# Performance work log

Hardware: AMD Instinct MI355X
Metric: run time of the kernel (lower is better)

Reference implementation:

```python
import jax, jax.numpy as jnp
import numpy as np

# FreeConv2D: locally-connected 2D conv (unshared per-location kernels) + bias.
# out[b,oh,ow,u] = sum_{i,j,c} w[oh,ow,u,i,j,c] * x[b, oh*s1+i, ow*s2+j, c] + bias[oh,ow,u]

B, H, W, C = 64, 64, 64, 64
U, K, S = 64, 5, 2
OH = (H - K) // S + 1  # 30 (== ceil((H-K+1)/S))
OW = (W - K) // S + 1  # 30


def setup_inputs() -> dict:
    key = jax.random.key(0)
    kx, kw, kb = jax.random.split(key, 3)
    x = jax.random.normal(kx, (B, H, W, C), dtype=jnp.float32)
    w = jax.random.normal(kw, (OH, OW, U, K, K, C), dtype=jnp.float32) * 0.05
    b = jax.random.normal(kb, (OH, OW, U), dtype=jnp.float32) * 0.05
    return {"x": x, "w": w, "b": b}


def reference(x, w, b):
    s1 = s2 = S
    # Accumulate over the small fixed kernel window (K*K = 25 taps);
    # each tap is a per-location contraction over channels (batched GEMV).
    out = jnp.zeros((x.shape[0], OH, OW, U), dtype=x.dtype)
    for i in range(K):
        for j in range(K):
            # x_slice[b,oh,ow,c] = x[b, oh*s1+i, ow*s2+j, c]
            x_slice = x[:, i:i + (OH - 1) * s1 + 1:s1, j:j + (OW - 1) * s2 + 1:s2, :]
            out = out + jnp.einsum('bhwc,hwuc->bhwu', x_slice, w[:, :, :, i, j, :])
    return out + b  # activation is None (identity)
```

## Files before the change

kernel.cpp:

```cpp
#include <hip/hip_runtime.h>


typedef __bf16 bf16x8 __attribute__((ext_vector_type(8)));
typedef float f32x4 __attribute__((ext_vector_type(4)));

__device__ __forceinline__ unsigned short f2bf(float f) {
    unsigned int u = __float_as_uint(f);
    u += 0x7FFFu + ((u >> 16) & 1u);
    return (unsigned short)(u >> 16);
}


__global__ __launch_bounds__(256, 4)
void freeconv_kernel(const float* __restrict__ x,
                     const float* __restrict__ w,
                     const float* __restrict__ bias,
                     float* __restrict__ out) {
    __shared__ __align__(16) unsigned short ldsA[10240];
    __shared__ __align__(16) unsigned short ldsB[10240];

    const int bid = blockIdx.x;
    const int oh = bid / 30;
    const int ow = bid - oh * 30;
    const int t = threadIdx.x;
    const int lane = t & 63;
    const int wave = t >> 6;
    const int wm = wave >> 1;
    const int wn = wave & 1;

    const int swz = ((lane >> 4) << 7) + (((lane & 15) ^ (lane >> 4)) << 3);

    int rr[10], cc[10], ww[10];
#pragma unroll
    for (int it = 0; it < 10; ++it) {
        int g = it * 256 + t;
        int r = g / 40;
        int k = (g - r * 40) * 4;
        rr[it] = r;
        cc[it] = k;
        int grp = (k >> 3) & 3;
        ww[it] = ((k >> 5) * 4 + (r >> 4)) * 512 + grp * 128 + (((r & 15) ^ grp) * 8) + (k & 7);
    }

    f32x4 acc[2][2];
#pragma unroll
    for (int a = 0; a < 2; ++a)
#pragma unroll
        for (int b2 = 0; b2 < 2; ++b2)
#pragma unroll
            for (int r = 0; r < 4; ++r) acc[a][b2][r] = 0.f;

    const float* wblk = w + (oh * 30 + ow) * 102400;

    for (int ci = 0; ci < 10; ++ci) {
        const int i  = ci >> 1;
        const int kh = ci & 1;
        const int aoff = (oh * 2 + i) * 4096 + ow * 128 + kh * 160;
        const int boff = i * 320 + kh * 160;

#pragma unroll
        for (int bt = 0; bt < 2; ++bt) {
            float4 va[5], vb[5];
#pragma unroll
            for (int q = 0; q < 5; ++q) {
                int it = bt * 5 + q;
                va[q] = *(const float4*)(x + rr[it] * 262144 + aoff + cc[it]);
            }
#pragma unroll
            for (int q = 0; q < 5; ++q) {
                int it = bt * 5 + q;
                vb[q] = *(const float4*)(wblk + rr[it] * 1600 + boff + cc[it]);
            }
#pragma unroll
            for (int q = 0; q < 5; ++q) {
                int it = bt * 5 + q;
                ushort4 pv;
                pv.x = f2bf(va[q].x); pv.y = f2bf(va[q].y);
                pv.z = f2bf(va[q].z); pv.w = f2bf(va[q].w);
                *(ushort4*)&ldsA[ww[it]] = pv;
            }
#pragma unroll
            for (int q = 0; q < 5; ++q) {
                int it = bt * 5 + q;
                ushort4 pv;
                pv.x = f2bf(vb[q].x); pv.y = f2bf(vb[q].y);
                pv.z = f2bf(vb[q].z); pv.w = f2bf(vb[q].w);
                *(ushort4*)&ldsB[ww[it]] = pv;
            }
        }
        __syncthreads();

#pragma unroll
        for (int ks = 0; ks < 5; ++ks) {
            const bf16x8 a0 = *(const bf16x8*)&ldsA[(ks * 4 + wm * 2 + 0) * 512 + swz];
            const bf16x8 a1 = *(const bf16x8*)&ldsA[(ks * 4 + wm * 2 + 1) * 512 + swz];
            const bf16x8 b0 = *(const bf16x8*)&ldsB[(ks * 4 + wn * 2 + 0) * 512 + swz];
            const bf16x8 b1 = *(const bf16x8*)&ldsB[(ks * 4 + wn * 2 + 1) * 512 + swz];
            acc[0][0] = __builtin_amdgcn_mfma_f32_16x16x32_bf16(a0, b0, acc[0][0], 0, 0, 0);
            acc[0][1] = __builtin_amdgcn_mfma_f32_16x16x32_bf16(a0, b1, acc[0][1], 0, 0, 0);
            acc[1][0] = __builtin_amdgcn_mfma_f32_16x16x32_bf16(a1, b0, acc[1][0], 0, 0, 0);
            acc[1][1] = __builtin_amdgcn_mfma_f32_16x16x32_bf16(a1, b1, acc[1][1], 0, 0, 0);
        }
        __syncthreads();
    }

    const float* bp = bias + (oh * 30 + ow) * 64;
    const int col = lane & 15;
    const int r0 = (lane >> 4) * 4;
    float bv0 = bp[wn * 32 + col];
    float bv1 = bp[wn * 32 + 16 + col];
#pragma unroll
    for (int ms = 0; ms < 2; ++ms) {
#pragma unroll
        for (int r = 0; r < 4; ++r) {
            int bi = wm * 32 + ms * 16 + r0 + r;
            float* op = out + ((bi * 30 + oh) * 30 + ow) * 64 + wn * 32 + col;
            op[0]  = acc[ms][0][r] + bv0;
            op[16] = acc[ms][1][r] + bv1;
        }
    }
}

extern "C" void kernel_launch(void* const* d_in, const int* in_sizes, int n_in,
                              void* d_out, int out_size, void* d_ws, size_t ws_size,
                              hipStream_t stream) {
    const float* x = (const float*)d_in[0];
    const float* w = (const float*)d_in[1];
    const float* b = (const float*)d_in[2];
    float* out = (float*)d_out;
    (void)in_sizes; (void)n_in; (void)out_size; (void)d_ws; (void)ws_size;
    freeconv_kernel<<<dim3(900), dim3(256), 0, stream>>>(x, w, b, out);
}
```

Measured before the change: 565.8 us.

## Prefetch next weight chunk in registers and remap blocks across XCDs

Weight tiles for the next chunk are loaded into registers while the current chunk's activation tile is converted and stored, overlapping the weight stream (the dominant traffic) with LDS writes and MFMA work. Block indices are remapped so neighbouring output locations land on the same XCD, which should improve L2 reuse of the overlapping input windows. Per-thread LDS address arrays are recomputed inline instead of held in registers. The change adds register pressure (20 float4 live values) under a 4-block occupancy bound, which could cause spills.

```diff
diff --git a/kernel.cpp b/kernel.cpp
--- a/kernel.cpp
+++ b/kernel.cpp
@@ -10,6 +10,12 @@
     return (unsigned short)(u >> 16);
 }
 
+__device__ __forceinline__ ushort4 pk4(const float4 v) {
+    ushort4 p;
+    p.x = f2bf(v.x); p.y = f2bf(v.y); p.z = f2bf(v.z); p.w = f2bf(v.w);
+    return p;
+}
+
 
 __global__ __launch_bounds__(256, 4)
 void freeconv_kernel(const float* __restrict__ x,
@@ -19,7 +25,12 @@
     __shared__ __align__(16) unsigned short ldsA[10240];
     __shared__ __align__(16) unsigned short ldsB[10240];
 
-    const int bid = blockIdx.x;
+    const int orig = blockIdx.x;
+    const int xcd  = orig & 7;
+    const int idx  = orig >> 3;
+    const int bid  = (xcd < 4) ? (xcd * 113 + idx)
+                               : (452 + (xcd - 4) * 112 + idx);
+
     const int oh = bid / 30;
     const int ow = bid - oh * 30;
     const int t = threadIdx.x;
@@ -30,17 +41,10 @@
 
     const int swz = ((lane >> 4) << 7) + (((lane & 15) ^ (lane >> 4)) << 3);
 
-    int rr[10], cc[10], ww[10];
+    int rr[10];
 #pragma unroll
-    for (int it = 0; it < 10; ++it) {
-        int g = it * 256 + t;
-        int r = g / 40;
-        int k = (g - r * 40) * 4;
-        rr[it] = r;
-        cc[it] = k;
-        int grp = (k >> 3) & 3;
-        ww[it] = ((k >> 5) * 4 + (r >> 4)) * 512 + grp * 128 + (((r & 15) ^ grp) * 8) + (k & 7);
-    }
+    for (int q = 0; q < 10; ++q) rr[q] = (q * 256 + t) / 40;
+    const int t4 = t << 2;
 
     f32x4 acc[2][2];
 #pragma unroll
@@ -50,44 +54,54 @@
 #pragma unroll
             for (int r = 0; r < 4; ++r) acc[a][b2][r] = 0.f;
 
-    const float* wblk = w + (oh * 30 + ow) * 102400;
+    const float* wblk = w + (size_t)bid * 102400;
+
+    float4 vb[10];
+#pragma unroll
+    for (int q = 0; q < 10; ++q) {
+        const int cc = q * 1024 + t4 - rr[q] * 160;
+        vb[q] = *(const float4*)(wblk + rr[q] * 1600 + cc);
+    }
 
     for (int ci = 0; ci < 10; ++ci) {
         const int i  = ci >> 1;
         const int kh = ci & 1;
         const int aoff = (oh * 2 + i) * 4096 + ow * 128 + kh * 160;
-        const int boff = i * 320 + kh * 160;
+
+        float4 va[10];
+#pragma unroll
+        for (int q = 0; q < 10; ++q) {
+            const int cc = q * 1024 + t4 - rr[q] * 160;
+            va[q] = *(const float4*)(x + rr[q] * 262144 + aoff + cc);
+        }
 
 #pragma unroll
-        for (int bt = 0; bt < 2; ++bt) {
-            float4 va[5], vb[5];
+        for (int q = 0; q < 10; ++q) {
+            const int cc  = q * 1024 + t4 - rr[q] * 160;
+            const int grp = (cc >> 3) & 3;
+            const int wv  = ((cc >> 5) * 4 + (rr[q] >> 4)) * 512 + grp * 128
+                          + (((rr[q] & 15) ^ grp) << 3) + (cc & 7);
+            *(ushort4*)&ldsB[wv] = pk4(vb[q]);
+        }
+
+        if (ci < 9) {
+            const int boff2 = ((ci + 1) >> 1) * 320 + ((ci + 1) & 1) * 160;
 #pragma unroll
-            for (int q = 0; q < 5; ++q) {
-                int it = bt * 5 + q;
-                va[q] = *(const float4*)(x + rr[it] * 262144 + aoff + cc[it]);
-            }
-#pragma unroll
-            for (int q = 0; q < 5; ++q) {
-                int it = bt * 5 + q;
-                vb[q] = *(const float4*)(wblk + rr[it] * 1600 + boff + cc[it]);
-            }
-#pragma unroll
-            for (int q = 0; q < 5; ++q) {
-                int it = bt * 5 + q;
-                ushort4 pv;
-                pv.x = f2bf(va[q].x); pv.y = f2bf(va[q].y);
-                pv.z = f2bf(va[q].z); pv.w = f2bf(va[q].w);
-                *(ushort4*)&ldsA[ww[it]] = pv;
-            }
-#pragma unroll
-            for (int q = 0; q < 5; ++q) {
-                int it = bt * 5 + q;
-                ushort4 pv;
-                pv.x = f2bf(vb[q].x); pv.y = f2bf(vb[q].y);
-                pv.z = f2bf(vb[q].z); pv.w = f2bf(vb[q].w);
-                *(ushort4*)&ldsB[ww[it]] = pv;
+            for (int q = 0; q < 10; ++q) {
+                const int cc = q * 1024 + t4 - rr[q] * 160;
+                vb[q] = *(const float4*)(wblk + rr[q] * 1600 + boff2 + cc);
             }
         }
+
+#pragma unroll
+        for (int q = 0; q < 10; ++q) {
+            const int cc  = q * 1024 + t4 - rr[q] * 160;
+            const int grp = (cc >> 3) & 3;
+            const int wv  = ((cc >> 5) * 4 + (rr[q] >> 4)) * 512 + grp * 128
+                          + (((rr[q] & 15) ^ grp) << 3) + (cc & 7);
+            *(ushort4*)&ldsA[wv] = pk4(va[q]);
+        }
+
         __syncthreads();
 
 #pragma unroll
@@ -101,20 +115,21 @@
             acc[1][0] = __builtin_amdgcn_mfma_f32_16x16x32_bf16(a1, b0, acc[1][0], 0, 0, 0);
             acc[1][1] = __builtin_amdgcn_mfma_f32_16x16x32_bf16(a1, b1, acc[1][1], 0, 0, 0);
         }
+
         __syncthreads();
     }
 
-    const float* bp = bias + (oh * 30 + ow) * 64;
+    const float* bp = bias + (size_t)bid * 64;
     const int col = lane & 15;
     const int r0 = (lane >> 4) * 4;
-    float bv0 = bp[wn * 32 + col];
-    float bv1 = bp[wn * 32 + 16 + col];
+    const float bv0 = bp[wn * 32 + col];
+    const float bv1 = bp[wn * 32 + 16 + col];
 #pragma unroll
     for (int ms = 0; ms < 2; ++ms) {
 #pragma unroll
         for (int r = 0; r < 4; ++r) {
-            int bi = wm * 32 + ms * 16 + r0 + r;
-            float* op = out + ((bi * 30 + oh) * 30 + ow) * 64 + wn * 32 + col;
+            const int bi = wm * 32 + ms * 16 + r0 + r;
+            float* op = out + ((size_t)(bi * 30 + oh) * 30 + ow) * 64 + wn * 32 + col;
             op[0]  = acc[ms][0][r] + bv0;
             op[16] = acc[ms][1][r] + bv1;
         }
```

Measured after the change: 664.1 us. 1.17x slower.
